# Optimization experiments

Hardware: AMD Instinct MI355X
Metric: run time of the kernel (lower is better)

## Reference

```python
import jax, jax.numpy as jnp
import numpy as np

NQ, NK = 32, 128  # local window sizes from AttentionIndex defaults
N_HEADS = 8


def _build_index(M):
    """Precompute block-sparse local attention indices (static, numpy).
    Returns query_idx [C,NQ], query_mask [C,NQ], key_idx [C,NK], key_mask [C,NK].
    """
    C = (M + NQ - 1) // NQ
    half = (NQ - 1.0) * 0.5
    centers = np.round(np.arange(half, M + half, NQ, dtype=np.float32)).astype(np.int64)
    q_idx = np.arange(C * NQ, dtype=np.int64)
    q_mask = q_idx < M
    q_idx = np.where(q_mask, q_idx, 0).reshape(C, NQ)
    q_mask = q_mask.reshape(C, NQ)
    key_idx = np.zeros((C, NK), np.int64)
    key_mask = np.zeros((C, NK), bool)
    for i, c in enumerate(centers):
        s = max(int(c) - NK // 2, 0)
        e = min(int(c) + NK // 2, M)
        w = e - s
        key_idx[i, :w] = np.arange(s, e, dtype=np.int64)
        key_mask[i, :w] = True
    return (jnp.asarray(q_idx), jnp.asarray(q_mask),
            jnp.asarray(key_idx), jnp.asarray(key_mask))


def setup_inputs() -> dict:
    key = jax.random.key(0)
    ks = jax.random.split(key, 6)
    B, M, D, N = 2, 16384, 256, 2048
    f_atom = jax.random.normal(ks[0], (B, M, D), jnp.float32)
    atom_mask = jnp.ones((B, M), jnp.float32)
    atom_token_uid = jnp.sort(jax.random.randint(ks[1], (B, M), 0, N), axis=-1)
    scale = 1.0 / np.sqrt(D)
    Wq = jax.random.normal(ks[2], (D, D), jnp.float32) * scale
    Wk = jax.random.normal(ks[3], (D, D), jnp.float32) * scale
    Wv = jax.random.normal(ks[4], (D, D), jnp.float32) * scale
    Wo = jax.random.normal(ks[5], (D, D), jnp.float32) * scale
    return {"f_atom": f_atom, "atom_mask": atom_mask, "Wq": Wq, "Wk": Wk,
            "Wv": Wv, "Wo": Wo, "atom_token_uid": atom_token_uid, "n_token": N}


def reference(f_atom, atom_mask, Wq, Wk, Wv, Wo, atom_token_uid, n_token):
    B, M, D = f_atom.shape
    H = N_HEADS
    dh = D // H
    q_idx, q_mask, k_idx, k_mask = _build_index(M)
    C = q_idx.shape[0]

    # projections -> [B,M,H,dh]
    q = (f_atom @ Wq).reshape(B, M, H, dh)
    k = (f_atom @ Wk).reshape(B, M, H, dh)
    v = (f_atom @ Wv).reshape(B, M, H, dh)

    # gather into local windows: queries [B,C,NQ,H,dh], keys/values [B,C,NK,H,dh]
    qb = q[:, q_idx]
    kb = k[:, k_idx]
    vb = v[:, k_idx]

    key_valid = (atom_mask[:, k_idx] > 0) & k_mask[None]            # [B,C,NK]
    alpha_mask = q_mask[None, None, :, :, None] & key_valid[:, None, :, None, :]  # [B,H,C,NQ,NK] (bcast)

    scores = jnp.einsum('bcqhd,bckhd->bhcqk', qb, kb) / np.sqrt(dh)  # [B,H,C,NQ,NK]
    scores = jnp.where(alpha_mask, scores, jnp.float32(-1e9))
    attn = jax.nn.softmax(scores, axis=-1)

    out = jnp.einsum('bhcqk,bckhd->bcqhd', attn, vb)                 # [B,C,NQ,H,dh]
    out = out.reshape(B, C * NQ, D)[:, :M] @ Wo                      # scatter back to [B,M,D]
    out = out * atom_mask[..., None]

    # aggregate atom feats -> token feats (masked segment mean), pad to n_token
    def agg(data, seg, mask):
        s = jax.ops.segment_sum(data * mask[:, None], seg, num_segments=n_token)
        cnt = jax.ops.segment_sum(mask, seg, num_segments=n_token)
        return s / (cnt[:, None] + 1e-8)

    f_token = jax.vmap(agg)(out, atom_token_uid, atom_mask)          # [B,N,D]
    return f_token
```

## Files before the change

kernel.cpp:

```cpp
#include <hip/hip_runtime.h>

typedef _Float16 f16;
typedef _Float16 f16x4 __attribute__((ext_vector_type(4)));
typedef _Float16 f16x8 __attribute__((ext_vector_type(8)));
typedef float    f32x16 __attribute__((ext_vector_type(16)));

#define MFMA(a, b, c) __builtin_amdgcn_mfma_f32_32x32x16_f16((a), (b), (c), 0, 0, 0)

static constexpr int Mg   = 16384;
static constexpr int Bg   = 2;
static constexpr int Dg   = 256;
static constexpr int Hg   = 8;
static constexpr int Cg   = 512;
static constexpr int Ntok = 2048;
static constexpr float QSCALE = 0.17677669529663687f;

typedef __attribute__((address_space(1))) const void gbl_cv;
typedef __attribute__((address_space(3))) void lds_v;

static __device__ __forceinline__ void gll16(const f16* g, f16* l) {
    __builtin_amdgcn_global_load_lds((gbl_cv*)g, (lds_v*)l, 16, 0, 0);
}
static __device__ __forceinline__ f16x8 mk8(f16x4 a, f16x4 b) {
    f16x8 r;
    r[0] = a[0]; r[1] = a[1]; r[2] = a[2]; r[3] = a[3];
    r[4] = b[0]; r[5] = b[1]; r[6] = b[2]; r[7] = b[3];
    return r;
}

__global__ __launch_bounds__(256) void k_wt(const float* __restrict__ Wq,
                                            const float* __restrict__ Wk,
                                            const float* __restrict__ Wv,
                                            const float* __restrict__ Wo,
                                            f16* __restrict__ Wsw) {
    int idx = blockIdx.x * 256 + threadIdx.x;
    int w   = idx >> 16;
    int rem = idx & 65535;
    int k   = rem >> 8;
    int n   = rem & 255;
    const float* W = (w == 0) ? Wq : (w == 1) ? Wk : (w == 2) ? Wv : Wo;
    int G = (k >> 3) ^ (n & 7);
    Wsw[w * 65536 + n * 256 + (G << 3) + (k & 7)] = (f16)W[k * 256 + n];
}

__global__ __launch_bounds__(256, 2) void k_qkv(const float* __restrict__ A,
                                                const f16* __restrict__ Wsw,
                                                f16* __restrict__ Qo,
                                                f16* __restrict__ Ko,
                                                f16* __restrict__ VT) {
    __shared__ f16 Ls[2][32 * 256];

    const int tid  = threadIdx.x;
    const int d    = blockIdx.x;
    const int lin  = (d & 7) * 64 + (d >> 3);
    const int yt   = lin >> 1;
    const int half = lin & 1;
    const int m0   = yt * 128;
    const int lane = tid & 63, w = tid >> 6;
    const int l31  = lane & 31, hi = lane >> 5;
    const int mrow = m0 + 32 * w + l31;
    const int xr   = l31 & 7;

    f16x8 a[16];
    const float* ap = A + (size_t)mrow * 256 + 8 * hi;
#pragma unroll
    for (int g = 0; g < 16; ++g) {
        float4 v0 = *reinterpret_cast<const float4*>(ap + 16 * g);
        float4 v1 = *reinterpret_cast<const float4*>(ap + 16 * g + 4);
        f16x8 t;
        t[0] = (f16)v0.x; t[1] = (f16)v0.y; t[2] = (f16)v0.z; t[3] = (f16)v0.w;
        t[4] = (f16)v1.x; t[5] = (f16)v1.y; t[6] = (f16)v1.z; t[7] = (f16)v1.w;
        a[g] = t;
    }

#define STW(S, BB)                                                             \
    {                                                                          \
        const f16* src = Wsw + ((S) >> 3) * 65536 + (((S) & 7) * 32) * 256;    \
        _Pragma("unroll")                                                      \
        for (int i = 0; i < 4; ++i) {                                          \
            int g2 = i * 256 + tid;                                            \
            gll16(src + g2 * 8, &Ls[BB][g2 * 8]);                              \
        }                                                                      \
    }

#define QKV_STEP(S, BB)                                                        \
    {                                                                          \
        if ((S) + 1 < s_end) { STW((S) + 1, (BB) ^ 1); }                       \
        f32x16 acc;                                                            \
        _Pragma("unroll")                                                      \
        for (int e = 0; e < 16; ++e) acc[e] = 0.f;                             \
        _Pragma("unroll")                                                      \
        for (int g = 0; g < 16; ++g) {                                         \
            f16x8 bf = *(const f16x8*)&Ls[BB][l31 * 256 +                      \
                                             (((2 * g + hi) ^ xr) << 3)];      \
            acc = MFMA(a[g], bf, acc);                                         \
        }                                                                      \
        const int wix  = (S) >> 3;                                             \
        const int gcol = ((S) & 7) * 32 + l31;                                 \
        const int mb   = m0 + 32 * w + 4 * hi;                                 \
        if (wix == 0) {                                                        \
            _Pragma("unroll")                                                  \
            for (int r = 0; r < 16; ++r)                                       \
                Qo[(size_t)(mb + (r & 3) + 8 * (r >> 2)) * 256 + gcol] =       \
                    (f16)(acc[r] * QSCALE);                                    \
        } else if (wix == 1) {                                                 \
            _Pragma("unroll")                                                  \
            for (int r = 0; r < 16; ++r)                                       \
                Ko[(size_t)(mb + (r & 3) + 8 * (r >> 2)) * 256 + gcol] =       \
                    (f16)acc[r];                                               \
        } else {                                                               \
            _Pragma("unroll")                                                  \
            for (int rq = 0; rq < 4; ++rq) {                                   \
                f16x4 pv = { (f16)acc[rq * 4 + 0], (f16)acc[rq * 4 + 1],       \
                             (f16)acc[rq * 4 + 2], (f16)acc[rq * 4 + 3] };     \
                int mr = mb + 8 * rq;                                          \
                int bb2 = mr >> 14, mm = mr & 16383;                           \
                *reinterpret_cast<f16x4*>(VT + (size_t)bb2 * (256 * 16384) +   \
                                          (size_t)gcol * 16384 + mm) = pv;     \
            }                                                                  \
        }                                                                      \
        if ((S) + 1 < s_end) {                                                 \
            if (((S) >> 3) == 2) {                                             \
                asm volatile("s_waitcnt vmcnt(4)" ::: "memory");               \
            } else {                                                           \
                asm volatile("s_waitcnt vmcnt(16)" ::: "memory");              \
            }                                                                  \
            __builtin_amdgcn_s_barrier();                                      \
            __builtin_amdgcn_sched_barrier(0);                                 \
        }                                                                      \
    }

#define QKV_RUN(BASE)                                                          \
    {                                                                          \
        const int s_end = (BASE) + 12;                                         \
        STW(BASE, 0);                                                          \
        asm volatile("s_waitcnt vmcnt(0)" ::: "memory");                       \
        __builtin_amdgcn_s_barrier();                                          \
        __builtin_amdgcn_sched_barrier(0);                                     \
        _Pragma("unroll")                                                      \
        for (int ss = 0; ss < 12; ++ss) { QKV_STEP((BASE) + ss, ss & 1); }     \
    }

    if (half == 0) { QKV_RUN(0); } else { QKV_RUN(12); }
#undef QKV_RUN
#undef QKV_STEP
#undef STW
}

__global__ __launch_bounds__(64) void k_attn(const f16* __restrict__ Qo,
                                             const f16* __restrict__ Ko,
                                             const f16* __restrict__ VT,
                                             f16* __restrict__ AO) {
    __shared__ f16 Vs[4096];

    const int tid = threadIdx.x;
    const int idx = blockIdx.x;
    const int lin = (idx & 7) * 1024 + (idx >> 3);
    const int h = lin & 7;
    const int c = (lin >> 3) & 511;
    const int b = lin >> 12;
    const int l31 = tid & 31, hi = tid >> 5;

    const int u0 = 32 * c - 48;
    const int e0 = (32 * c + 80 < Mg) ? (32 * c + 80) : Mg;

    const f16* Vb = VT + (size_t)b * Dg * Mg + (size_t)h * 32 * Mg;
#pragma unroll
    for (int i = 0; i < 8; ++i) {
        int seg = 2 * i + hi;
        int m0s = u0 + 8 * seg;
        if (m0s < 0) m0s = 0;
        if (m0s > Mg - 8) m0s = Mg - 8;
        gll16(Vb + (size_t)l31 * Mg + m0s, &Vs[i * 512 + tid * 8]);
    }

    const f16* qp = Qo + ((size_t)b * Mg + 32 * c + l31) * 256 + h * 32;
    f16x8 qf0 = *reinterpret_cast<const f16x8*>(qp + 8 * hi);
    f16x8 qf1 = *reinterpret_cast<const f16x8*>(qp + 16 + 8 * hi);

    f32x16 p4[4];
#pragma unroll
    for (int t = 0; t < 4; ++t)
#pragma unroll
        for (int e = 0; e < 16; ++e) p4[t][e] = 0.f;

#pragma unroll
    for (int t = 0; t < 4; ++t) {
        int grow = u0 + 32 * t + l31;
        int grc  = grow < 0 ? 0 : (grow > Mg - 1 ? Mg - 1 : grow);
        const f16* kp = Ko + ((size_t)b * Mg + grc) * 256 + h * 32;
        f16x8 kf0 = *reinterpret_cast<const f16x8*>(kp + 8 * hi);
        f16x8 kf1 = *reinterpret_cast<const f16x8*>(kp + 16 + 8 * hi);
        p4[t] = MFMA(kf0, qf0, p4[t]);
        p4[t] = MFMA(kf1, qf1, p4[t]);
    }

    float mx = -3e38f;
#pragma unroll
    for (int t = 0; t < 4; ++t)
#pragma unroll
        for (int r = 0; r < 16; ++r) {
            int gm = u0 + 32 * t + (r & 3) + 8 * (r >> 2) + 4 * hi;
            if (gm >= 0 && gm < e0) mx = fmaxf(mx, p4[t][r]);
        }
    mx = fmaxf(mx, __shfl_xor(mx, 32));

    float sum = 0.f;
#pragma unroll
    for (int t = 0; t < 4; ++t)
#pragma unroll
        for (int r = 0; r < 16; ++r) {
            int gm = u0 + 32 * t + (r & 3) + 8 * (r >> 2) + 4 * hi;
            float ev = (gm >= 0 && gm < e0) ? __expf(p4[t][r] - mx) : 0.f;
            p4[t][r] = ev;
            sum += ev;
        }
    sum += __shfl_xor(sum, 32);
    const float inv = 1.f / sum;
#pragma unroll
    for (int t = 0; t < 4; ++t)
#pragma unroll
        for (int e = 0; e < 16; ++e) p4[t][e] *= inv;

    asm volatile("s_waitcnt vmcnt(0)" ::: "memory");
    __builtin_amdgcn_sched_barrier(0);

    f32x16 o;
#pragma unroll
    for (int e = 0; e < 16; ++e) o[e] = 0.f;

#pragma unroll
    for (int s = 0; s < 8; ++s) {
        f16x8 pa;
#pragma unroll
        for (int e = 0; e < 8; ++e) pa[e] = (f16)(p4[s >> 1][8 * (s & 1) + e]);
        f16x4 v0 = *reinterpret_cast<const f16x4*>(&Vs[(2 * s) * 256 + l31 * 8 + 4 * hi]);
        f16x4 v1 = *reinterpret_cast<const f16x4*>(&Vs[(2 * s + 1) * 256 + l31 * 8 + 4 * hi]);
        o = MFMA(pa, mk8(v0, v1), o);
    }

#pragma unroll
    for (int r = 0; r < 16; ++r) {
        int mrow = 32 * c + (r & 3) + 8 * (r >> 2) + 4 * hi;
        AO[((size_t)b * Mg + mrow) * 256 + h * 32 + l31] = (f16)o[r];
    }
}

__global__ __launch_bounds__(256, 2) void k_out(const f16* __restrict__ AO,
                                                const f16* __restrict__ Wsw,
                                                f16* __restrict__ OUT) {
    __shared__ f16 Ls[2][32 * 256];

    const int tid  = threadIdx.x;
    const int d    = blockIdx.x;
    const int lin  = (d & 7) * 64 + (d >> 3);
    const int yt   = lin >> 1;
    const int half = lin & 1;
    const int m0   = yt * 128;
    const int lane = tid & 63, w = tid >> 6;
    const int l31  = lane & 31, hi = lane >> 5;
    const int mrow = m0 + 32 * w + l31;
    const int xr   = l31 & 7;

    f16x8 a[16];
    const f16* ap = AO + (size_t)mrow * 256 + 8 * hi;
#pragma unroll
    for (int g = 0; g < 16; ++g)
        a[g] = *reinterpret_cast<const f16x8*>(ap + 16 * g);

#define STW(S, BB)                                                             \
    {                                                                          \
        const f16* src = Wsw + 3 * 65536 + ((S) * 32) * 256;                   \
        _Pragma("unroll")                                                      \
        for (int i = 0; i < 4; ++i) {                                          \
            int g2 = i * 256 + tid;                                            \
            gll16(src + g2 * 8, &Ls[BB][g2 * 8]);                              \
        }                                                                      \
    }

    const int s_base = half * 4;
    STW(s_base, 0);
    asm volatile("s_waitcnt vmcnt(0)" ::: "memory");
    __builtin_amdgcn_s_barrier();
    __builtin_amdgcn_sched_barrier(0);

#pragma unroll
    for (int ss = 0; ss < 4; ++ss) {
        const int S  = s_base + ss;
        const int BB = ss & 1;
        if (ss + 1 < 4) { STW(S + 1, BB ^ 1); }
        f32x16 acc;
#pragma unroll
        for (int e = 0; e < 16; ++e) acc[e] = 0.f;
#pragma unroll
        for (int g = 0; g < 16; ++g) {
            f16x8 bf = *(const f16x8*)&Ls[BB][l31 * 256 + (((2 * g + hi) ^ xr) << 3)];
            acc = MFMA(a[g], bf, acc);
        }
        const int gcol = S * 32 + l31;
        const int mb   = m0 + 32 * w + 4 * hi;
#pragma unroll
        for (int r = 0; r < 16; ++r)
            OUT[(size_t)(mb + (r & 3) + 8 * (r >> 2)) * 256 + gcol] = (f16)acc[r];
        if (ss + 1 < 4) {
            asm volatile("s_waitcnt vmcnt(16)" ::: "memory");
            __builtin_amdgcn_s_barrier();
            __builtin_amdgcn_sched_barrier(0);
        }
    }
#undef STW
}

__global__ __launch_bounds__(256) void k_seg(const f16* __restrict__ OUT,
                                             const int* __restrict__ uid,
                                             const float* __restrict__ mask,
                                             float* __restrict__ out) {
    const int t = blockIdx.x, b = blockIdx.y;
    const int d = threadIdx.x;
    const int* u = uid + b * Mg;

    int lo = 0, hi = Mg;
    while (lo < hi) { int mid = (lo + hi) >> 1; if (u[mid] < t) lo = mid + 1; else hi = mid; }
    int lo2 = lo, hi2 = Mg;
    while (lo2 < hi2) { int mid = (lo2 + hi2) >> 1; if (u[mid] < t + 1) lo2 = mid + 1; else hi2 = mid; }

    float sum = 0.f, cnt = 0.f;
    for (int m = lo; m < lo2; ++m) {
        float msk = mask[b * Mg + m];
        sum += msk * msk * (float)OUT[((size_t)b * Mg + m) * 256 + d];
        cnt += msk;
    }
    out[((size_t)b * Ntok + t) * 256 + d] = sum / (cnt + 1e-8f);
}

extern "C" void kernel_launch(void* const* d_in, const int* in_sizes, int n_in,
                              void* d_out, int out_size, void* d_ws, size_t ws_size,
                              hipStream_t stream) {
    const float* f_atom = (const float*)d_in[0];
    const float* amask  = (const float*)d_in[1];
    const float* Wq     = (const float*)d_in[2];
    const float* Wk     = (const float*)d_in[3];
    const float* Wv     = (const float*)d_in[4];
    const float* Wo     = (const float*)d_in[5];
    const int*   uid    = (const int*)d_in[6];

    const size_t HALF_WT  = 4 * 65536;
    const size_t HALF_MAT = (size_t)Bg * Mg * Dg;
    const size_t needed_bytes = (HALF_WT + 5 * HALF_MAT) * sizeof(f16);
    if (ws_size < needed_bytes) return;

    f16* Wsw  = (f16*)d_ws;
    f16* Qb   = Wsw + HALF_WT;
    f16* Kb   = Qb + HALF_MAT;
    f16* VTb  = Kb + HALF_MAT;
    f16* AOb  = VTb + HALF_MAT;
    f16* OUTb = AOb + HALF_MAT;

    k_wt  <<<dim3(1024), 256, 0, stream>>>(Wq, Wk, Wv, Wo, Wsw);
    k_qkv <<<dim3(512), 256, 0, stream>>>(f_atom, Wsw, Qb, Kb, VTb);
    k_attn<<<dim3(8192), 64, 0, stream>>>(Qb, Kb, VTb, AOb);
    k_out <<<dim3(512), 256, 0, stream>>>(AOb, Wsw, OUTb);
    k_seg <<<dim3(Ntok, Bg), 256, 0, stream>>>(OUTb, uid, amask, (float*)d_out);
}
```

Before: 91.07 us.

## Fuse attention and output projection into one kernel via LDS-staged AO tile

```diff
diff --git a/kernel.cpp b/kernel.cpp
--- a/kernel.cpp
+++ b/kernel.cpp
@@ -147,23 +147,27 @@
 #undef STW
 }
 
-__global__ __launch_bounds__(64) void k_attn(const f16* __restrict__ Qo,
-                                             const f16* __restrict__ Ko,
-                                             const f16* __restrict__ VT,
-                                             f16* __restrict__ AO) {
-    __shared__ f16 Vs[4096];
-
-    const int tid = threadIdx.x;
-    const int idx = blockIdx.x;
-    const int lin = (idx & 7) * 1024 + (idx >> 3);
-    const int h = lin & 7;
-    const int c = (lin >> 3) & 511;
-    const int b = lin >> 12;
-    const int l31 = tid & 31, hi = tid >> 5;
+__global__ __launch_bounds__(512, 4) void k_attn(const f16* __restrict__ Qo,
+                                                 const f16* __restrict__ Ko,
+                                                 const f16* __restrict__ VT,
+                                                 const f16* __restrict__ Wsw,
+                                                 f16* __restrict__ OUT) {
+    __shared__ f16 Vs[8 * 4096];
+    __shared__ f16 AOs[32 * 256];
+
+    const int tid  = threadIdx.x;
+    const int idx  = blockIdx.x;
+    const int lin  = (idx & 7) * 128 + (idx >> 3);
+    const int b    = lin >> 9;
+    const int c    = lin & 511;
+    const int h    = tid >> 6;
+    const int lane = tid & 63;
+    const int l31  = lane & 31, hi = lane >> 5;
 
     const int u0 = 32 * c - 48;
     const int e0 = (32 * c + 80 < Mg) ? (32 * c + 80) : Mg;
 
+    f16* Vw = Vs + h * 4096;
     const f16* Vb = VT + (size_t)b * Dg * Mg + (size_t)h * 32 * Mg;
 #pragma unroll
     for (int i = 0; i < 8; ++i) {
@@ -171,7 +175,7 @@
         int m0s = u0 + 8 * seg;
         if (m0s < 0) m0s = 0;
         if (m0s > Mg - 8) m0s = Mg - 8;
-        gll16(Vb + (size_t)l31 * Mg + m0s, &Vs[i * 512 + tid * 8]);
+        gll16(Vb + (size_t)l31 * Mg + m0s, &Vw[i * 512 + lane * 8]);
     }
 
     const f16* qp = Qo + ((size_t)b * Mg + 32 * c + l31) * 256 + h * 32;
@@ -234,81 +238,42 @@
         f16x8 pa;
 #pragma unroll
         for (int e = 0; e < 8; ++e) pa[e] = (f16)(p4[s >> 1][8 * (s & 1) + e]);
-        f16x4 v0 = *reinterpret_cast<const f16x4*>(&Vs[(2 * s) * 256 + l31 * 8 + 4 * hi]);
-        f16x4 v1 = *reinterpret_cast<const f16x4*>(&Vs[(2 * s + 1) * 256 + l31 * 8 + 4 * hi]);
+        f16x4 v0 = *reinterpret_cast<const f16x4*>(&Vw[(2 * s) * 256 + l31 * 8 + 4 * hi]);
+        f16x4 v1 = *reinterpret_cast<const f16x4*>(&Vw[(2 * s + 1) * 256 + l31 * 8 + 4 * hi]);
         o = MFMA(pa, mk8(v0, v1), o);
     }
 
-#pragma unroll
-    for (int r = 0; r < 16; ++r) {
-        int mrow = 32 * c + (r & 3) + 8 * (r >> 2) + 4 * hi;
-        AO[((size_t)b * Mg + mrow) * 256 + h * 32 + l31] = (f16)o[r];
-    }
-}
-
-__global__ __launch_bounds__(256, 2) void k_out(const f16* __restrict__ AO,
-                                                const f16* __restrict__ Wsw,
-                                                f16* __restrict__ OUT) {
-    __shared__ f16 Ls[2][32 * 256];
-
-    const int tid  = threadIdx.x;
-    const int d    = blockIdx.x;
-    const int lin  = (d & 7) * 64 + (d >> 3);
-    const int yt   = lin >> 1;
-    const int half = lin & 1;
-    const int m0   = yt * 128;
-    const int lane = tid & 63, w = tid >> 6;
-    const int l31  = lane & 31, hi = lane >> 5;
-    const int mrow = m0 + 32 * w + l31;
-    const int xr   = l31 & 7;
-
-    f16x8 a[16];
-    const f16* ap = AO + (size_t)mrow * 256 + 8 * hi;
-#pragma unroll
-    for (int g = 0; g < 16; ++g)
-        a[g] = *reinterpret_cast<const f16x8*>(ap + 16 * g);
-
-#define STW(S, BB)                                                             \
-    {                                                                          \
-        const f16* src = Wsw + 3 * 65536 + ((S) * 32) * 256;                   \
-        _Pragma("unroll")                                                      \
-        for (int i = 0; i < 4; ++i) {                                          \
-            int g2 = i * 256 + tid;                                            \
-            gll16(src + g2 * 8, &Ls[BB][g2 * 8]);                              \
-        }                                                                      \
-    }
-
-    const int s_base = half * 4;
-    STW(s_base, 0);
-    asm volatile("s_waitcnt vmcnt(0)" ::: "memory");
-    __builtin_amdgcn_s_barrier();
-    __builtin_amdgcn_sched_barrier(0);
-
-#pragma unroll
-    for (int ss = 0; ss < 4; ++ss) {
-        const int S  = s_base + ss;
-        const int BB = ss & 1;
-        if (ss + 1 < 4) { STW(S + 1, BB ^ 1); }
+    {
+        const int col = h * 32 + l31;
+        const int cg  = col >> 3;
+        const int c7  = col & 7;
+#pragma unroll
+        for (int r = 0; r < 16; ++r) {
+            int row = (r & 3) + 8 * (r >> 2) + 4 * hi;
+            AOs[row * 256 + ((cg ^ (row & 7)) << 3) + c7] = (f16)o[r];
+        }
+    }
+    __syncthreads();
+
+    {
+        const int xr = l31 & 7;
+        const f16* Wb = Wsw + 3 * 65536 + (size_t)(h * 32 + l31) * 256;
         f32x16 acc;
 #pragma unroll
         for (int e = 0; e < 16; ++e) acc[e] = 0.f;
 #pragma unroll
         for (int g = 0; g < 16; ++g) {
-            f16x8 bf = *(const f16x8*)&Ls[BB][l31 * 256 + (((2 * g + hi) ^ xr) << 3)];
-            acc = MFMA(a[g], bf, acc);
-        }
-        const int gcol = S * 32 + l31;
-        const int mb   = m0 + 32 * w + 4 * hi;
-#pragma unroll
-        for (int r = 0; r < 16; ++r)
-            OUT[(size_t)(mb + (r & 3) + 8 * (r >> 2)) * 256 + gcol] = (f16)acc[r];
-        if (ss + 1 < 4) {
-            asm volatile("s_waitcnt vmcnt(16)" ::: "memory");
-            __builtin_amdgcn_s_barrier();
-            __builtin_amdgcn_sched_barrier(0);
-        }
-    }
-#undef STW
+            int gp = (2 * g + hi) ^ xr;
+            f16x8 av = *(const f16x8*)&AOs[l31 * 256 + (gp << 3)];
+            f16x8 bv = *(const f16x8*)(Wb + (gp << 3));
+            acc = MFMA(av, bv, acc);
+        }
+#pragma unroll
+        for (int r = 0; r < 16; ++r) {
+            int row = (r & 3) + 8 * (r >> 2) + 4 * hi;
+            OUT[((size_t)b * Mg + 32 * c + row) * 256 + h * 32 + l31] = (f16)acc[r];
+        }
+    }
 }
 
 __global__ __launch_bounds__(256) void k_seg(const f16* __restrict__ OUT,
@@ -346,19 +311,17 @@
 
     const size_t HALF_WT  = 4 * 65536;
     const size_t HALF_MAT = (size_t)Bg * Mg * Dg;
-    const size_t needed_bytes = (HALF_WT + 5 * HALF_MAT) * sizeof(f16);
+    const size_t needed_bytes = (HALF_WT + 4 * HALF_MAT) * sizeof(f16);
     if (ws_size < needed_bytes) return;
 
     f16* Wsw  = (f16*)d_ws;
     f16* Qb   = Wsw + HALF_WT;
     f16* Kb   = Qb + HALF_MAT;
     f16* VTb  = Kb + HALF_MAT;
-    f16* AOb  = VTb + HALF_MAT;
-    f16* OUTb = AOb + HALF_MAT;
+    f16* OUTb = VTb + HALF_MAT;
 
     k_wt  <<<dim3(1024), 256, 0, stream>>>(Wq, Wk, Wv, Wo, Wsw);
     k_qkv <<<dim3(512), 256, 0, stream>>>(f_atom, Wsw, Qb, Kb, VTb);
-    k_attn<<<dim3(8192), 64, 0, stream>>>(Qb, Kb, VTb, AOb);
-    k_out <<<dim3(512), 256, 0, stream>>>(AOb, Wsw, OUTb);
+    k_attn<<<dim3(1024), 512, 0, stream>>>(Qb, Kb, VTb, Wsw, OUTb);
     k_seg <<<dim3(Ntok, Bg), 256, 0, stream>>>(OUTb, uid, amask, (float*)d_out);
 }
```

New measurement: 88.35 us. 1.03x faster.
